# Kernel optimization log

Hardware: AMD Instinct MI355X
Metric: run time of the kernel (lower is better)

## Reference

```python
import jax, jax.numpy as jnp
from jax import lax
import numpy as np

N, C, T, V = 32, 64, 300, 25   # batch, channels, frames, joints
INTER = 16                     # out_channels // coff_embedding (64//4)
NS = 3                         # num_subset
K = 9                          # temporal kernel size
EPS = 1e-5                     # torch BatchNorm2d default eps


def _bn(x, g, b):
    # training-mode BatchNorm2d over (N, T, V) per channel, biased variance
    m = x.mean(axis=(0, 2, 3), keepdims=True)
    v = x.var(axis=(0, 2, 3), keepdims=True)
    return (x - m) * lax.rsqrt(v + EPS) * g[None, :, None, None] + b[None, :, None, None]


def setup_inputs() -> dict:
    key = jax.random.key(0)
    ks = jax.random.split(key, 8)
    rn = lambda k, shape, sc=0.05: jax.random.normal(k, shape, jnp.float32) * sc
    x = jax.random.normal(ks[0], (N, C, T, V), jnp.float32)
    A = jax.random.uniform(ks[1], (NS, V, V), dtype=jnp.float32)
    PA = jnp.full((NS, V, V), 1e-6, jnp.float32)   # learned adjacency offset (init 1e-6)
    Wa = rn(ks[2], (NS, INTER, C)); ba = jnp.zeros((NS, INTER), jnp.float32)
    Wb = rn(ks[3], (NS, INTER, C)); bb = jnp.zeros((NS, INTER), jnp.float32)
    Wd = rn(ks[4], (NS, C, C));     bd = jnp.zeros((NS, C), jnp.float32)
    g1 = jnp.ones((C,), jnp.float32); b1 = jnp.zeros((C,), jnp.float32)
    Wt = rn(ks[5], (C, C, K, 1));   bt = jnp.zeros((C,), jnp.float32)
    g2 = jnp.ones((C,), jnp.float32); b2 = jnp.zeros((C,), jnp.float32)
    return dict(x=x, A=A, PA=PA, Wa=Wa, ba=ba, Wb=Wb, bb=bb, Wd=Wd, bd=bd,
                g1=g1, b1=b1, Wt=Wt, bt=bt, g2=g2, b2=b2)


def reference(x, A, PA, Wa, ba, Wb, bb, Wd, bd, g1, b1, Wt, bt, g2, b2):
    n, c, t, v = x.shape
    Au = A + PA                      # effective adjacency per subset, [NS,V,V]
    scale = 1.0 / (INTER * t)        # A1.size(-1)
    x_flat = x.reshape(n, c * t, v)  # [N, C*T, V]
    y = None
    for i in range(NS):
        # 1x1 convs -> embeddings, [N, INTER, T, V]
        a = jnp.einsum('nctv,oc->notv', x, Wa[i]) + ba[i][None, :, None, None]
        b = jnp.einsum('nctv,oc->notv', x, Wb[i]) + bb[i][None, :, None, None]
        A1 = a.transpose(0, 3, 1, 2).reshape(n, v, INTER * t)  # [N, V, INTER*T]
        A2 = b.reshape(n, INTER * t, v)                        # [N, INTER*T, V]
        attn = jax.nn.softmax(jnp.matmul(A1, A2) * scale, axis=-2) + Au[i]  # [N,V,V]
        z = jnp.matmul(x_flat, attn).reshape(n, c, t, v)       # aggregate over joints
        z = jnp.einsum('nctv,oc->notv', z, Wd[i]) + bd[i][None, :, None, None]
        y = z if y is None else y + z
    y = jax.nn.relu(_bn(y, g1, b1) + x)      # gcn bn + identity down + relu
    # temporal conv (9,1), pad (4,0), stride 1, then BN
    yc = lax.conv_general_dilated(y, Wt, window_strides=(1, 1),
                                  padding=((K // 2, K // 2), (0, 0)),
                                  dimension_numbers=('NCHW', 'OIHW', 'NCHW'))
    yc = _bn(yc + bt[None, :, None, None], g2, b2)
    return jax.nn.relu(yc + x)               # identity residual (in==out, stride 1)
```

## Files before the change

### kernel.cpp

```cpp
#include <hip/hip_runtime.h>
#include <hip/hip_bf16.h>

#define NB 32
#define CH 64
#define TF 300
#define VJ 25
#define NSUB 3
#define ICB 16
#define KW 9
#define EPSB 1e-5f

#define TVsz (TF*VJ)
#define CTVsz (CH*TF*VJ)
#define TOTAL (NB*CTVsz)
#define PCCOUNT (NB*TF*VJ)

#define ATC 32
#define ATCN 10

typedef __attribute__((ext_vector_type(8))) short s16x8;
typedef __attribute__((ext_vector_type(4))) float f32x4;

__device__ __forceinline__ unsigned short f2bf(float v) {
    __hip_bfloat16 h = __float2bfloat16(v);
    return *(unsigned short*)&h;
}
__device__ __forceinline__ float bf2f(unsigned int u) {
    return __uint_as_float(u << 16);
}

__global__ void k_prep(const float* __restrict__ Wt, const float* __restrict__ Wd,
                       const float* __restrict__ Wa, const float* __restrict__ ba,
                       const float* __restrict__ Wb, const float* __restrict__ bb,
                       unsigned short* __restrict__ awT, unsigned short* __restrict__ wdcat,
                       unsigned short* __restrict__ wcat, float* __restrict__ biascat) {
    int e = blockIdx.x * 256 + threadIdx.x;
    if (e < CH*CH*KW) {
        int o = e / (CH*KW), c = (e / KW) % CH, k = e % KW;
        awT[(k*CH + o)*CH + c] = f2bf(Wt[e]);
        return;
    }
    int e2 = e - CH*CH*KW;
    if (e2 < NSUB*CH*CH) { wdcat[e2] = f2bf(Wd[e2]); return; }
    int e3 = e2 - NSUB*CH*CH;
    if (e3 < 6144) {
        int i = e3 / 2048, rm = (e3 >> 6) & 31, c = e3 & 63;
        wcat[e3] = f2bf((rm < 16) ? Wa[(i*ICB + rm)*CH + c] : Wb[(i*ICB + rm - 16)*CH + c]);
        return;
    }
    if (e3 < 6240) {
        int j = e3 - 6144;
        int i = j >> 5, r = j & 31;
        biascat[j] = (r < 16) ? ba[i*ICB + r] : bb[i*ICB + r - 16];
    }
}

__global__ __launch_bounds__(256) void k_xt(const float* __restrict__ x,
                                            unsigned short* __restrict__ xbt,
                                            unsigned short* __restrict__ xbc) {
    __shared__ unsigned short ls[64*66];
    int b = blockIdx.x;
    int n = b / 118, tile = b % 118;
    int tv0 = tile * 64;
    int tid = threadIdx.x;
    const float* xg = x + (long)n * CTVsz;
    for (int e = tid; e < 1024; e += 256) {
        int c = e >> 4, t4 = (e & 15) * 4;
        int tv = tv0 + t4;
        if (tv < TVsz) {
            float4 v = *(const float4*)(xg + (long)c*TVsz + tv);
            unsigned short h0 = f2bf(v.x), h1 = f2bf(v.y), h2 = f2bf(v.z), h3 = f2bf(v.w);
            ls[(t4+0)*66 + c] = h0;
            ls[(t4+1)*66 + c] = h1;
            ls[(t4+2)*66 + c] = h2;
            ls[(t4+3)*66 + c] = h3;
            *(uint2*)&xbc[((long)n*CH + c)*TVsz + tv] =
                make_uint2((unsigned)h0 | ((unsigned)h1 << 16),
                           (unsigned)h2 | ((unsigned)h3 << 16));
        }
    }
    __syncthreads();
    for (int e = tid; e < 1024; e += 256) {
        int tvl = e >> 4, c4 = (e & 15) * 4;
        int tv = tv0 + tvl;
        if (tv < TVsz) {
            unsigned int lo = *(const unsigned int*)&ls[tvl*66 + c4];
            unsigned int hi = *(const unsigned int*)&ls[tvl*66 + c4 + 2];
            *(uint2*)&xbt[((long)n*TVsz + tv)*CH + c4] = make_uint2(lo, hi);
        }
    }
}

__global__ __launch_bounds__(256) void k_attn(
    const unsigned short* __restrict__ xbt, const unsigned short* __restrict__ wcat,
    const float* __restrict__ biascat, float* __restrict__ Mbuf)
{
    __shared__ __align__(16) char emb[32*32*ATC*2];
    __shared__ float gram[625];
    int b = blockIdx.x;
    int i   = b / (NB*ATCN);
    int rem = b % (NB*ATCN);
    int n = rem / ATCN, tc = rem % ATCN;
    int t0 = tc * ATC;
    int tid = threadIdx.x;
    int wv = tid >> 6, l = tid & 63, l15 = l & 15, lhi = l >> 4;

    for (int e = tid; e < 625; e += 256) gram[e] = 0.f;

    s16x8 wf[2][2];
    #pragma unroll
    for (int mf = 0; mf < 2; ++mf)
        #pragma unroll
        for (int kc = 0; kc < 2; ++kc)
            wf[mf][kc] = *(const s16x8*)(wcat + ((i*32 + mf*16 + l15)*64 + kc*32 + lhi*8));
    float bs[2][4];
    #pragma unroll
    for (int mf = 0; mf < 2; ++mf)
        #pragma unroll
        for (int r = 0; r < 4; ++r)
            bs[mf][r] = biascat[i*32 + mf*16 + lhi*4 + r];

    const unsigned short* xb = xbt + (long)n * TVsz * CH;
    for (int v = wv; v < 25; v += 4) {
        f32x4 ae[2][2];
        #pragma unroll
        for (int mf = 0; mf < 2; ++mf)
            #pragma unroll
            for (int nf = 0; nf < 2; ++nf)
                ae[mf][nf] = (f32x4){0.f,0.f,0.f,0.f};
        #pragma unroll
        for (int nf = 0; nf < 2; ++nf) {
            int t = t0 + nf*16 + l15;
            int tcl = t < TF ? t : TF-1;
            const unsigned short* bp = xb + ((long)tcl*VJ + v)*CH;
            s16x8 b0 = *(const s16x8*)(bp + lhi*8);
            s16x8 b1 = *(const s16x8*)(bp + 32 + lhi*8);
            #pragma unroll
            for (int mf = 0; mf < 2; ++mf) {
                ae[mf][nf] = __builtin_amdgcn_mfma_f32_16x16x32_bf16(wf[mf][0], b0, ae[mf][nf], 0,0,0);
                ae[mf][nf] = __builtin_amdgcn_mfma_f32_16x16x32_bf16(wf[mf][1], b1, ae[mf][nf], 0,0,0);
            }
        }
        #pragma unroll
        for (int mf = 0; mf < 2; ++mf)
            #pragma unroll
            for (int nf = 0; nf < 2; ++nf)
                #pragma unroll
                for (int r = 0; r < 4; ++r) {
                    int t  = t0 + nf*16 + l15;
                    int tl = nf*16 + l15;
                    int m  = mf*16 + lhi*4 + r;
                    float val = (t < TF) ? (ae[mf][nf][r] + bs[mf][r]) : 0.f;
                    int byte = (((v*32 + m)*ATC + tl)*2) ^ ((v&7)<<4);
                    *(unsigned short*)(emb + byte) = f2bf(val);
                }
    }
    __syncthreads();

    f32x4 ag[2][2];
    #pragma unroll
    for (int mu = 0; mu < 2; ++mu)
        #pragma unroll
        for (int nw = 0; nw < 2; ++nw)
            ag[mu][nw] = (f32x4){0.f,0.f,0.f,0.f};
    #pragma unroll
    for (int oo = 0; oo < 4; ++oo) {
        int o = wv*4 + oo;
        s16x8 fa[2], fb[2];
        #pragma unroll
        for (int mu = 0; mu < 2; ++mu) {
            int u = mu*16 + l15; if (u > 24) u = 24;
            fa[mu] = *(const s16x8*)(emb + ((((u*32 + o)*ATC + lhi*8)*2) ^ ((u&7)<<4)));
        }
        #pragma unroll
        for (int nw = 0; nw < 2; ++nw) {
            int w = nw*16 + l15; if (w > 24) w = 24;
            fb[nw] = *(const s16x8*)(emb + ((((w*32 + 16 + o)*ATC + lhi*8)*2) ^ ((w&7)<<4)));
        }
        #pragma unroll
        for (int mu = 0; mu < 2; ++mu)
            #pragma unroll
            for (int nw = 0; nw < 2; ++nw)
                ag[mu][nw] = __builtin_amdgcn_mfma_f32_16x16x32_bf16(fa[mu], fb[nw], ag[mu][nw], 0,0,0);
    }
    #pragma unroll
    for (int mu = 0; mu < 2; ++mu)
        #pragma unroll
        for (int nw = 0; nw < 2; ++nw)
            #pragma unroll
            for (int r = 0; r < 4; ++r) {
                int u = mu*16 + lhi*4 + r;
                int w = nw*16 + l15;
                if (u < 25 && w < 25)
                    atomicAdd(&gram[u*25 + w], ag[mu][nw][r]);
            }
    __syncthreads();
    for (int e = tid; e < 625; e += 256)
        atomicAdd(&Mbuf[(i*NB + n)*625 + e], gram[e]);
}

__global__ void k_softmax(const float* __restrict__ A, const float* __restrict__ PA,
                          float* __restrict__ Mbuf) {
    int b = blockIdx.x;
    int i = b / NB;
    int w = threadIdx.x;
    if (w >= 25) return;
    float* M = Mbuf + b*625;
    const float scale = 1.0f / (float)(ICB * TF);
    float col[25];
    float mx = -1e30f;
    #pragma unroll
    for (int u = 0; u < 25; ++u) { col[u] = M[u*25 + w] * scale; mx = fmaxf(mx, col[u]); }
    float s = 0.f;
    #pragma unroll
    for (int u = 0; u < 25; ++u) { col[u] = __expf(col[u] - mx); s += col[u]; }
    float inv = 1.0f / s;
    #pragma unroll
    for (int u = 0; u < 25; ++u)
        M[u*25 + w] = col[u]*inv + A[i*625 + u*25 + w] + PA[i*625 + u*25 + w];
}

__global__ __launch_bounds__(256) void k_yz(
    const unsigned short* __restrict__ xbc, const float* __restrict__ Mbuf,
    const unsigned short* __restrict__ wdcat, const float* __restrict__ bd,
    unsigned short* __restrict__ ybuf, float* __restrict__ s1, float* __restrict__ s2)
{
    __shared__ __align__(16) unsigned short attnT[NSUB][32][40];
    __shared__ __align__(16) char zT[4][32*144];
    __shared__ float ss[64], sq[64];

    int b = blockIdx.x;
    int n = b / 75, tq = b % 75;
    int tid = threadIdx.x;
    int wv = tid >> 6, l = tid & 63, l15 = l & 15, lhi = l >> 4;

    if (tid < 64) { ss[tid] = 0.f; sq[tid] = 0.f; }
    for (int e = tid; e < NSUB*32*40; e += 256) {
        int i = e / 1280, r = e % 1280, v = r / 40, u = r % 40;
        ((unsigned short*)attnT)[e] =
            (v < 25 && u < 25) ? f2bf(Mbuf[(i*NB + n)*625 + u*25 + v]) : (unsigned short)0;
    }
    __syncthreads();

    char* z = zT[wv];
    unsigned short* zp = (unsigned short*)z;
    int tg = tq*4 + wv;

    const unsigned short* xr = xbc + (long)n*CTVsz + tg*25;
    s16x8 bf1[4];
    #pragma unroll
    for (int nf = 0; nf < 4; ++nf)
        bf1[nf] = *(const s16x8*)(xr + (long)(nf*16 + l15)*TVsz + lhi*8);

    f32x4 acc2[4][2];
    #pragma unroll
    for (int mf = 0; mf < 4; ++mf)
        #pragma unroll
        for (int nf = 0; nf < 2; ++nf)
            acc2[mf][nf] = (f32x4){0.f,0.f,0.f,0.f};

    const f32x4 z4 = (f32x4){0.f,0.f,0.f,0.f};
    for (int i = 0; i < NSUB; ++i) {
        s16x8 af1[2];
        #pragma unroll
        for (int mf = 0; mf < 2; ++mf)
            af1[mf] = *(const s16x8*)((const char*)attnT + i*2560 + (mf*16 + l15)*80 + lhi*16);
        f32x4 a1[2][4];
        #pragma unroll
        for (int nf = 0; nf < 4; ++nf)
            #pragma unroll
            for (int mf = 0; mf < 2; ++mf)
                a1[mf][nf] = __builtin_amdgcn_mfma_f32_16x16x32_bf16(af1[mf], bf1[nf], z4, 0,0,0);
        #pragma unroll
        for (int mf = 0; mf < 2; ++mf)
            #pragma unroll
            for (int nf = 0; nf < 4; ++nf)
                #pragma unroll
                for (int r = 0; r < 4; ++r)
                    zp[(mf*16 + lhi*4 + r)*72 + nf*16 + l15] = f2bf(a1[mf][nf][r]);
        #pragma unroll
        for (int kc = 0; kc < 2; ++kc) {
            s16x8 bf2[2];
            #pragma unroll
            for (int nf = 0; nf < 2; ++nf)
                bf2[nf] = *(const s16x8*)(z + (nf*16 + l15)*144 + kc*64 + lhi*16);
            #pragma unroll
            for (int mf = 0; mf < 4; ++mf) {
                s16x8 af2 = *(const s16x8*)(wdcat + ((i*CH + mf*16 + l15)*CH + kc*32 + lhi*8));
                #pragma unroll
                for (int nf = 0; nf < 2; ++nf)
                    acc2[mf][nf] = __builtin_amdgcn_mfma_f32_16x16x32_bf16(af2, bf2[nf], acc2[mf][nf], 0,0,0);
            }
        }
    }

    #pragma unroll
    for (int mf = 0; mf < 4; ++mf) {
        #pragma unroll
        for (int r = 0; r < 4; ++r) {
            int o = mf*16 + lhi*4 + r;
            float bds = bd[o] + bd[CH + o] + bd[2*CH + o];
            float p = 0.f, q = 0.f;
            #pragma unroll
            for (int nf = 0; nf < 2; ++nf) {
                int v = nf*16 + l15;
                if (v < VJ) {
                    float val = acc2[mf][nf][r] + bds;
                    ybuf[((long)n*CH + o)*TVsz + tg*25 + v] = f2bf(val);
                    p += val; q += val*val;
                }
            }
            p += __shfl_xor(p, 1, 64); q += __shfl_xor(q, 1, 64);
            p += __shfl_xor(p, 2, 64); q += __shfl_xor(q, 2, 64);
            p += __shfl_xor(p, 4, 64); q += __shfl_xor(q, 4, 64);
            p += __shfl_xor(p, 8, 64); q += __shfl_xor(q, 8, 64);
            if (l15 == 0) { atomicAdd(&ss[o], p); atomicAdd(&sq[o], q); }
        }
    }
    __syncthreads();
    if (tid < 64) { atomicAdd(&s1[tid], ss[tid]); atomicAdd(&s2[tid], sq[tid]); }
}

__global__ __launch_bounds__(256) void k_bn1t(
    const float* __restrict__ x, const float* __restrict__ g1, const float* __restrict__ b1,
    const float* __restrict__ s1, const float* __restrict__ s2,
    const unsigned short* __restrict__ yb, unsigned short* __restrict__ ybt)
{
    __shared__ unsigned short ls[64*66];
    int b = blockIdx.x;
    int n = b / 118, tile = b % 118;
    int tv0 = tile * 64;
    const float invN = 1.0f / (float)PCCOUNT;
    int tid = threadIdx.x;

    for (int e = tid; e < 1024; e += 256) {
        int c = e >> 4, t4 = (e & 15) * 4;
        int tv = tv0 + t4;
        if (tv < TVsz) {
            long gbase = (long)n*CTVsz + (long)c*TVsz;
            float m  = s1[c] * invN;
            float vr = s2[c] * invN - m*m;
            float sc = rsqrtf(vr + EPSB) * g1[c];
            float bc = b1[c];
            uint2 yv = *(const uint2*)(yb + gbase + tv);
            float4 xv = *(const float4*)(x + gbase + tv);
            ls[(t4+0)*66 + c] = f2bf(fmaxf((bf2f(yv.x & 0xffffu) - m)*sc + bc + xv.x, 0.f));
            ls[(t4+1)*66 + c] = f2bf(fmaxf((bf2f(yv.x >> 16)     - m)*sc + bc + xv.y, 0.f));
            ls[(t4+2)*66 + c] = f2bf(fmaxf((bf2f(yv.y & 0xffffu) - m)*sc + bc + xv.z, 0.f));
            ls[(t4+3)*66 + c] = f2bf(fmaxf((bf2f(yv.y >> 16)     - m)*sc + bc + xv.w, 0.f));
        }
    }
    __syncthreads();
    for (int e = tid; e < 1024; e += 256) {
        int tvl = e >> 4, c4 = (e & 15) * 4;
        int tv = tv0 + tvl;
        if (tv < TVsz) {
            int v = tv % 25, t = tv / 25;
            unsigned int lo = *(const unsigned int*)&ls[tvl*66 + c4];
            unsigned int hi = *(const unsigned int*)&ls[tvl*66 + c4 + 2];
            *(uint2*)&ybt[(((long)n*VJ + v)*TF + t)*CH + c4] = make_uint2(lo, hi);
        }
    }
}

#define TCROWS 316

__global__ __launch_bounds__(256) void k_tconv(
    const unsigned short* __restrict__ ybt, const unsigned short* __restrict__ awT,
    const float* __restrict__ bt, unsigned short* __restrict__ ycb,
    float* __restrict__ s1, float* __restrict__ s2)
{
    __shared__ __align__(16) char ys[TCROWS*128];
    __shared__ float ss[64], sq[64];
    int b = blockIdx.x;
    int n = b / VJ, v = b % VJ;
    int tid = threadIdx.x;
    int wv = tid >> 6, l = tid & 63, l15 = l & 15, lhi = l >> 4;
    if (tid < 64) { ss[tid] = 0.f; sq[tid] = 0.f; }

    const char* src = (const char*)(ybt + (((long)n*VJ + v)*TF)*CH);
    for (int qq = tid; qq < TCROWS*8; qq += 256) {
        int row = qq >> 3;
        int cb  = (qq & 7) << 4;
        int tg = row - 4;
        uint4 val = make_uint4(0u,0u,0u,0u);
        if (tg >= 0 && tg < TF)
            val = *(const uint4*)(src + (long)tg*128 + cb);
        *(uint4*)(ys + row*128 + (cb ^ ((row & 7) << 4))) = val;
    }
    __syncthreads();

    int wt0 = wv * 75;
    const short* aw = (const short*)awT;

    f32x4 acc[4][5];
    #pragma unroll
    for (int mf = 0; mf < 4; ++mf)
        #pragma unroll
        for (int nf = 0; nf < 5; ++nf)
            acc[mf][nf] = (f32x4){0.f,0.f,0.f,0.f};

    for (int tap = 0; tap < KW; ++tap) {
        #pragma unroll
        for (int kc = 0; kc < 2; ++kc) {
            s16x8 af[4], bfr[5];
            #pragma unroll
            for (int mf = 0; mf < 4; ++mf)
                af[mf] = *(const s16x8*)(aw + ((tap*CH + mf*16 + l15)*CH + kc*32 + lhi*8));
            #pragma unroll
            for (int nf = 0; nf < 5; ++nf) {
                int rloc = wt0 + nf*16 + l15 + tap;
                int cb = (kc*64 + lhi*16) ^ ((rloc & 7) << 4);
                bfr[nf] = *(const s16x8*)(ys + rloc*128 + cb);
            }
            #pragma unroll
            for (int mf = 0; mf < 4; ++mf)
                #pragma unroll
                for (int nf = 0; nf < 5; ++nf)
                    acc[mf][nf] = __builtin_amdgcn_mfma_f32_16x16x32_bf16(
                        af[mf], bfr[nf], acc[mf][nf], 0, 0, 0);
        }
    }

    #pragma unroll
    for (int mf = 0; mf < 4; ++mf) {
        #pragma unroll
        for (int r = 0; r < 4; ++r) {
            int o = mf*16 + lhi*4 + r;
            float bo = bt[o];
            float p = 0.f, q = 0.f;
            #pragma unroll
            for (int nf = 0; nf < 5; ++nf) {
                int tle = nf*16 + l15;
                if (tle < 75) {
                    float val = acc[mf][nf][r] + bo;
                    ycb[(((long)n*CH + o)*VJ + v)*TF + wt0 + tle] = f2bf(val);
                    p += val; q += val*val;
                }
            }
            p += __shfl_xor(p, 1, 64); q += __shfl_xor(q, 1, 64);
            p += __shfl_xor(p, 2, 64); q += __shfl_xor(q, 2, 64);
            p += __shfl_xor(p, 4, 64); q += __shfl_xor(q, 4, 64);
            p += __shfl_xor(p, 8, 64); q += __shfl_xor(q, 8, 64);
            if (l15 == 0) { atomicAdd(&ss[o], p); atomicAdd(&sq[o], q); }
        }
    }
    __syncthreads();
    if (tid < 64) { atomicAdd(&s1[tid], ss[tid]); atomicAdd(&s2[tid], sq[tid]); }
}

__global__ __launch_bounds__(256) void k_out(
    const float* __restrict__ x, const float* __restrict__ g2, const float* __restrict__ b2,
    const float* __restrict__ s1, const float* __restrict__ s2,
    const unsigned short* __restrict__ ycb, float* __restrict__ out)
{
    __shared__ float ls[VJ*305];
    const float invN = 1.0f / (float)PCCOUNT;
    int b = blockIdx.x;
    int n = b >> 6, c = b & 63;
    int tid = threadIdx.x;

    float m  = s1[c] * invN;
    float vr = s2[c] * invN - m*m;
    float rs = rsqrtf(vr + EPSB) * g2[c];
    float bc = b2[c];

    const uint2* yc = (const uint2*)(ycb + ((long)n*CH + c)*TVsz);
    for (int e = tid; e < TVsz/4; e += 256) {
        uint2 d = yc[e];
        int base = e*4;
        int v = base / TF, t = base % TF;
        float* lp = &ls[v*305 + t];
        lp[0] = (bf2f(d.x & 0xffffu) - m)*rs + bc;
        lp[1] = (bf2f(d.x >> 16)     - m)*rs + bc;
        lp[2] = (bf2f(d.y & 0xffffu) - m)*rs + bc;
        lp[3] = (bf2f(d.y >> 16)     - m)*rs + bc;
    }
    __syncthreads();

    long gbase = ((long)n*CH + c)*TVsz;
    for (int e = tid; e < TVsz/4; e += 256) {
        int tv = e*4;
        float4 xv = *(const float4*)(x + gbase + tv);
        float4 ov;
        { int v = (tv+0) % 25, t = (tv+0) / 25; ov.x = fmaxf(ls[v*305 + t] + xv.x, 0.f); }
        { int v = (tv+1) % 25, t = (tv+1) / 25; ov.y = fmaxf(ls[v*305 + t] + xv.y, 0.f); }
        { int v = (tv+2) % 25, t = (tv+2) / 25; ov.z = fmaxf(ls[v*305 + t] + xv.z, 0.f); }
        { int v = (tv+3) % 25, t = (tv+3) / 25; ov.w = fmaxf(ls[v*305 + t] + xv.w, 0.f); }
        *(float4*)(out + gbase + tv) = ov;
    }
}

extern "C" void kernel_launch(void* const* d_in, const int* in_sizes, int n_in,
                              void* d_out, int out_size, void* d_ws, size_t ws_size,
                              hipStream_t stream) {
    const float* x  = (const float*)d_in[0];
    const float* A  = (const float*)d_in[1];
    const float* PA = (const float*)d_in[2];
    const float* Wa = (const float*)d_in[3];
    const float* ba = (const float*)d_in[4];
    const float* Wb = (const float*)d_in[5];
    const float* bb = (const float*)d_in[6];
    const float* Wd = (const float*)d_in[7];
    const float* bd = (const float*)d_in[8];
    const float* g1 = (const float*)d_in[9];
    const float* b1 = (const float*)d_in[10];
    const float* Wt = (const float*)d_in[11];
    const float* bt = (const float*)d_in[12];
    const float* g2 = (const float*)d_in[13];
    const float* b2 = (const float*)d_in[14];

    float* ws    = (float*)d_ws;
    float* Mbuf  = ws;
    float* stats = ws + 60000;
    unsigned short* wdcat  = (unsigned short*)(ws + 60256);
    unsigned short* wcat   = (unsigned short*)(ws + 66400);
    float* biascat = ws + 69472;
    unsigned short* awT    = (unsigned short*)(ws + 69568);
    unsigned short* xbt    = (unsigned short*)(ws + 88000);
    unsigned short* xbc    = (unsigned short*)(ws + 7768000);
    unsigned short* ybuf   = (unsigned short*)(ws + 15448000);
    unsigned short* ybt = xbt;
    unsigned short* ycb = xbc;

    hipMemsetAsync(Mbuf, 0, (60000 + 256)*sizeof(float), stream);
    k_prep<<<217, 256, 0, stream>>>(Wt, Wd, Wa, ba, Wb, bb, awT, wdcat, wcat, biascat);
    k_xt<<<NB*118, 256, 0, stream>>>(x, xbt, xbc);
    k_attn<<<NSUB*NB*ATCN, 256, 0, stream>>>(xbt, wcat, biascat, Mbuf);
    k_softmax<<<NSUB*NB, 32, 0, stream>>>(A, PA, Mbuf);
    k_yz<<<NB*75, 256, 0, stream>>>(xbc, Mbuf, wdcat, bd, ybuf, stats, stats + 64);
    k_bn1t<<<NB*118, 256, 0, stream>>>(x, g1, b1, stats, stats + 64, ybuf, ybt);
    k_tconv<<<NB*VJ, 256, 0, stream>>>(ybt, awT, bt, ycb, stats + 128, stats + 192);
    k_out<<<NB*CH, 256, 0, stream>>>(x, g2, b2, stats + 128, stats + 192, ycb, (float*)d_out);
}
```

Before: 281.4 us.

## Pre-pack bf16 attention in softmax and keep intermediate z in registers via bpermute

The softmax kernel now writes the attention matrix directly as padded, transposed bf16 tiles, so each k_yz block just vector-copies it into shared memory instead of converting and transposing it from fp32 Mbuf. In k_yz, the first matmul is reoriented (x as the A operand, attention as B), and its result is passed to the second MFMA through ds_bpermute lane shuffles instead of a per-wave shared-memory staging buffer. This removes the LDS round trip and its store/load traffic for z, and shrinks LDS use, at the cost of extra permute instructions and more register pressure.

Result: faster. 270.4 us (-3.9%).

```diff
diff --git a/kernel.cpp b/kernel.cpp
--- a/kernel.cpp
+++ b/kernel.cpp
@@ -200,12 +200,20 @@
 }
 
 __global__ void k_softmax(const float* __restrict__ A, const float* __restrict__ PA,
-                          float* __restrict__ Mbuf) {
-    int b = blockIdx.x;
-    int i = b / NB;
+                          const float* __restrict__ Mbuf,
+                          unsigned short* __restrict__ attnbf) {
+    int b = blockIdx.x;
+    int i = b / NB, n = b % NB;
     int w = threadIdx.x;
-    if (w >= 25) return;
-    float* M = Mbuf + b*625;
+    unsigned short* row = attnbf + (((long)n*NSUB + i)*32 + w)*40;
+    if (w >= 25) {
+        if (w < 32) {
+            #pragma unroll
+            for (int u = 0; u < 40; ++u) row[u] = 0;
+        }
+        return;
+    }
+    const float* M = Mbuf + b*625;
     const float scale = 1.0f / (float)(ICB * TF);
     float col[25];
     float mx = -1e30f;
@@ -217,16 +225,17 @@
     float inv = 1.0f / s;
     #pragma unroll
     for (int u = 0; u < 25; ++u)
-        M[u*25 + w] = col[u]*inv + A[i*625 + u*25 + w] + PA[i*625 + u*25 + w];
+        row[u] = f2bf(col[u]*inv + A[i*625 + u*25 + w] + PA[i*625 + u*25 + w]);
+    #pragma unroll
+    for (int u = 25; u < 40; ++u) row[u] = 0;
 }
 
 __global__ __launch_bounds__(256) void k_yz(
-    const unsigned short* __restrict__ xbc, const float* __restrict__ Mbuf,
+    const unsigned short* __restrict__ xbc, const unsigned short* __restrict__ attnbf,
     const unsigned short* __restrict__ wdcat, const float* __restrict__ bd,
     unsigned short* __restrict__ ybuf, float* __restrict__ s1, float* __restrict__ s2)
 {
-    __shared__ __align__(16) unsigned short attnT[NSUB][32][40];
-    __shared__ __align__(16) char zT[4][32*144];
+    __shared__ __align__(16) unsigned short attnT[NSUB*32*40];
     __shared__ float ss[64], sq[64];
 
     int b = blockIdx.x;
@@ -235,22 +244,19 @@
     int wv = tid >> 6, l = tid & 63, l15 = l & 15, lhi = l >> 4;
 
     if (tid < 64) { ss[tid] = 0.f; sq[tid] = 0.f; }
-    for (int e = tid; e < NSUB*32*40; e += 256) {
-        int i = e / 1280, r = e % 1280, v = r / 40, u = r % 40;
-        ((unsigned short*)attnT)[e] =
-            (v < 25 && u < 25) ? f2bf(Mbuf[(i*NB + n)*625 + u*25 + v]) : (unsigned short)0;
-    }
-    __syncthreads();
-
-    char* z = zT[wv];
-    unsigned short* zp = (unsigned short*)z;
+    {
+        const uint4* srcp = (const uint4*)(attnbf + (long)n * (NSUB*32*40));
+        uint4* dstp = (uint4*)attnT;
+        for (int e = tid; e < 480; e += 256) dstp[e] = srcp[e];
+    }
+    __syncthreads();
+
     int tg = tq*4 + wv;
-
     const unsigned short* xr = xbc + (long)n*CTVsz + tg*25;
-    s16x8 bf1[4];
-    #pragma unroll
-    for (int nf = 0; nf < 4; ++nf)
-        bf1[nf] = *(const s16x8*)(xr + (long)(nf*16 + l15)*TVsz + lhi*8);
+    s16x8 afx[4];
+    #pragma unroll
+    for (int mf = 0; mf < 4; ++mf)
+        afx[mf] = *(const s16x8*)(xr + (long)(mf*16 + l15)*TVsz + lhi*8);
 
     f32x4 acc2[4][2];
     #pragma unroll
@@ -259,37 +265,59 @@
         for (int nf = 0; nf < 2; ++nf)
             acc2[mf][nf] = (f32x4){0.f,0.f,0.f,0.f};
 
-    const f32x4 z4 = (f32x4){0.f,0.f,0.f,0.f};
+    int srcA4 = (l15 + 32*(lhi & 1)) << 2;
+    int srcB4 = srcA4 + 64;
+    bool hsel = (lhi & 2) != 0;
+
+    const f32x4 zero4 = (f32x4){0.f,0.f,0.f,0.f};
     for (int i = 0; i < NSUB; ++i) {
-        s16x8 af1[2];
-        #pragma unroll
-        for (int mf = 0; mf < 2; ++mf)
-            af1[mf] = *(const s16x8*)((const char*)attnT + i*2560 + (mf*16 + l15)*80 + lhi*16);
-        f32x4 a1[2][4];
-        #pragma unroll
-        for (int nf = 0; nf < 4; ++nf)
-            #pragma unroll
-            for (int mf = 0; mf < 2; ++mf)
-                a1[mf][nf] = __builtin_amdgcn_mfma_f32_16x16x32_bf16(af1[mf], bf1[nf], z4, 0,0,0);
-        #pragma unroll
-        for (int mf = 0; mf < 2; ++mf)
-            #pragma unroll
-            for (int nf = 0; nf < 4; ++nf)
-                #pragma unroll
-                for (int r = 0; r < 4; ++r)
-                    zp[(mf*16 + lhi*4 + r)*72 + nf*16 + l15] = f2bf(a1[mf][nf][r]);
+        s16x8 bfa0 = *(const s16x8*)(attnT + (i*32 + l15)*40 + lhi*8);
+        s16x8 bfa1 = *(const s16x8*)(attnT + (i*32 + 16 + l15)*40 + lhi*8);
+        f32x4 zacc[4][2];
+        #pragma unroll
+        for (int mf = 0; mf < 4; ++mf) {
+            zacc[mf][0] = __builtin_amdgcn_mfma_f32_16x16x32_bf16(afx[mf], bfa0, zero4, 0,0,0);
+            zacc[mf][1] = __builtin_amdgcn_mfma_f32_16x16x32_bf16(afx[mf], bfa1, zero4, 0,0,0);
+        }
+        unsigned pk[4][2][2];
+        #pragma unroll
+        for (int mf = 0; mf < 4; ++mf)
+            #pragma unroll
+            for (int nf = 0; nf < 2; ++nf) {
+                pk[mf][nf][0] = (unsigned)f2bf(zacc[mf][nf][0]) | ((unsigned)f2bf(zacc[mf][nf][1]) << 16);
+                pk[mf][nf][1] = (unsigned)f2bf(zacc[mf][nf][2]) | ((unsigned)f2bf(zacc[mf][nf][3]) << 16);
+            }
         #pragma unroll
         for (int kc = 0; kc < 2; ++kc) {
-            s16x8 bf2[2];
-            #pragma unroll
-            for (int nf = 0; nf < 2; ++nf)
-                bf2[nf] = *(const s16x8*)(z + (nf*16 + l15)*144 + kc*64 + lhi*16);
-            #pragma unroll
-            for (int mf = 0; mf < 4; ++mf) {
-                s16x8 af2 = *(const s16x8*)(wdcat + ((i*CH + mf*16 + l15)*CH + kc*32 + lhi*8));
-                #pragma unroll
-                for (int nf = 0; nf < 2; ++nf)
-                    acc2[mf][nf] = __builtin_amdgcn_mfma_f32_16x16x32_bf16(af2, bf2[nf], acc2[mf][nf], 0,0,0);
+            s16x8 bz[2];
+            #pragma unroll
+            for (int nf = 0; nf < 2; ++nf) {
+                unsigned dw0, dw1, dw2, dw3;
+                {
+                    unsigned a0 = (unsigned)__builtin_amdgcn_ds_bpermute(srcA4, (int)pk[kc*2+0][nf][0]);
+                    unsigned a1 = (unsigned)__builtin_amdgcn_ds_bpermute(srcA4, (int)pk[kc*2+1][nf][0]);
+                    unsigned b0 = (unsigned)__builtin_amdgcn_ds_bpermute(srcB4, (int)pk[kc*2+0][nf][0]);
+                    unsigned b1 = (unsigned)__builtin_amdgcn_ds_bpermute(srcB4, (int)pk[kc*2+1][nf][0]);
+                    dw0 = hsel ? a1 : a0;
+                    dw2 = hsel ? b1 : b0;
+                }
+                {
+                    unsigned a0 = (unsigned)__builtin_amdgcn_ds_bpermute(srcA4, (int)pk[kc*2+0][nf][1]);
+                    unsigned a1 = (unsigned)__builtin_amdgcn_ds_bpermute(srcA4, (int)pk[kc*2+1][nf][1]);
+                    unsigned b0 = (unsigned)__builtin_amdgcn_ds_bpermute(srcB4, (int)pk[kc*2+0][nf][1]);
+                    unsigned b1 = (unsigned)__builtin_amdgcn_ds_bpermute(srcB4, (int)pk[kc*2+1][nf][1]);
+                    dw1 = hsel ? a1 : a0;
+                    dw3 = hsel ? b1 : b0;
+                }
+                union { s16x8 v; unsigned u[4]; } tmp;
+                tmp.u[0] = dw0; tmp.u[1] = dw1; tmp.u[2] = dw2; tmp.u[3] = dw3;
+                bz[nf] = tmp.v;
+            }
+            #pragma unroll
+            for (int mf2 = 0; mf2 < 4; ++mf2) {
+                s16x8 afw = *(const s16x8*)(wdcat + ((i*CH + mf2*16 + l15)*CH + kc*32 + lhi*8));
+                acc2[mf2][0] = __builtin_amdgcn_mfma_f32_16x16x32_bf16(afw, bz[0], acc2[mf2][0], 0,0,0);
+                acc2[mf2][1] = __builtin_amdgcn_mfma_f32_16x16x32_bf16(afw, bz[1], acc2[mf2][1], 0,0,0);
             }
         }
     }
@@ -513,13 +541,14 @@
     float* ws    = (float*)d_ws;
     float* Mbuf  = ws;
     float* stats = ws + 60000;
-    unsigned short* wdcat  = (unsigned short*)(ws + 60256);
-    unsigned short* wcat   = (unsigned short*)(ws + 66400);
-    float* biascat = ws + 69472;
-    unsigned short* awT    = (unsigned short*)(ws + 69568);
-    unsigned short* xbt    = (unsigned short*)(ws + 88000);
-    unsigned short* xbc    = (unsigned short*)(ws + 7768000);
-    unsigned short* ybuf   = (unsigned short*)(ws + 15448000);
+    unsigned short* attnbf = (unsigned short*)(ws + 60256);
+    unsigned short* wdcat  = (unsigned short*)(ws + 121696);
+    unsigned short* wcat   = (unsigned short*)(ws + 127840);
+    float* biascat = ws + 130912;
+    unsigned short* awT    = (unsigned short*)(ws + 131008);
+    unsigned short* xbt    = (unsigned short*)(ws + 149440);
+    unsigned short* xbc    = (unsigned short*)(ws + 7829440);
+    unsigned short* ybuf   = (unsigned short*)(ws + 15509440);
     unsigned short* ybt = xbt;
     unsigned short* ycb = xbc;
 
@@ -527,8 +556,8 @@
     k_prep<<<217, 256, 0, stream>>>(Wt, Wd, Wa, ba, Wb, bb, awT, wdcat, wcat, biascat);
     k_xt<<<NB*118, 256, 0, stream>>>(x, xbt, xbc);
     k_attn<<<NSUB*NB*ATCN, 256, 0, stream>>>(xbt, wcat, biascat, Mbuf);
-    k_softmax<<<NSUB*NB, 32, 0, stream>>>(A, PA, Mbuf);
-    k_yz<<<NB*75, 256, 0, stream>>>(xbc, Mbuf, wdcat, bd, ybuf, stats, stats + 64);
+    k_softmax<<<NSUB*NB, 32, 0, stream>>>(A, PA, Mbuf, attnbf);
+    k_yz<<<NB*75, 256, 0, stream>>>(xbc, attnbf, wdcat, bd, ybuf, stats, stats + 64);
     k_bn1t<<<NB*118, 256, 0, stream>>>(x, g1, b1, stats, stats + 64, ybuf, ybt);
     k_tconv<<<NB*VJ, 256, 0, stream>>>(ybt, awT, bt, ycb, stats + 128, stats + 192);
     k_out<<<NB*CH, 256, 0, stream>>>(x, g2, b2, stats + 128, stats + 192, ycb, (float*)d_out);
```
